# Performance work log

Measured on AMD Instinct MI355X. Metric: run time of the kernel, lower is better.

The kernel has to match this reference:

```python
import jax, jax.numpy as jnp
import numpy as np

B, S, D = 4, 2048, 1024
H, HD = 16, 64
WINDOW = 256


def setup_inputs() -> dict:
    key = jax.random.key(0)
    ks = jax.random.split(key, 5)
    scale = 1.0 / np.sqrt(D)
    return {
        "hidden_states": jax.random.normal(ks[0], (B, S, D), dtype=jnp.float32),
        "Wq": jax.random.normal(ks[1], (D, D), dtype=jnp.float32) * scale,
        "Wk": jax.random.normal(ks[2], (D, D), dtype=jnp.float32) * scale,
        "Wv": jax.random.normal(ks[3], (D, D), dtype=jnp.float32) * scale,
        "Wo": jax.random.normal(ks[4], (D, D), dtype=jnp.float32) * scale,
        "bo": jnp.zeros((D,), dtype=jnp.float32),
    }


def reference(hidden_states, Wq, Wk, Wv, Wo, bo):
    # q/k/v projections (no bias), torch Linear: x @ W.T
    q = hidden_states @ Wq.T  # [B,S,D]
    k = hidden_states @ Wk.T
    v = hidden_states @ Wv.T

    def split_heads(t):  # [B,S,D] -> [B,H,S,HD]
        return t.reshape(B, S, H, HD).transpose(0, 2, 1, 3)

    q, k, v = split_heads(q), split_heads(k), split_heads(v)

    # NOTE: original code does NOT scale by 1/sqrt(head_dim)
    scores = jnp.einsum("bhqd,bhkd->bhqk", q.astype(jnp.float32), k.astype(jnp.float32))

    # local causal band mask: keep j <= i and i - j < WINDOW
    i = jnp.arange(S)[:, None]
    j = jnp.arange(S)[None, :]
    band = (j <= i) & (i - j < WINDOW)  # [S,S] bool
    mask_value = jnp.finfo(scores.dtype).min
    scores = jnp.where(band[None, None, :, :], scores, mask_value)

    attn = jax.nn.softmax(scores, axis=-1).astype(v.dtype)
    ctx = jnp.einsum("bhqk,bhkd->bhqd", attn, v)  # [B,H,S,HD]

    # merge heads -> [B,S,D]
    ctx = ctx.transpose(0, 2, 1, 3).reshape(B, S, D)
    out = ctx @ Wo.T + bo
    return out
```

## Files before the change

kernel.cpp:

```cpp
#include <hip/hip_runtime.h>
#include <hip/hip_bf16.h>
#include <cstdint>
#include <cstddef>

#define S_LEN   2048
#define BATCH   4
#define NHEAD   16
#define HDIM    64
#define DMODEL  1024
#define WIN     256
#define PQ      72

typedef __bf16 bf16x8 __attribute__((ext_vector_type(8)));
typedef float f32x4 __attribute__((ext_vector_type(4)));
typedef unsigned short u16x4 __attribute__((ext_vector_type(4)));
typedef unsigned short u16x8 __attribute__((ext_vector_type(8)));

__device__ __forceinline__ unsigned short f2bf(float x) {
  union { float f; unsigned u; } c; c.f = x;
  unsigned r = (c.u + 0x7fffu + ((c.u >> 16) & 1u)) >> 16;
  return (unsigned short)r;
}

__device__ __forceinline__ void gld_lds16(const void* g, void* l) {
  __builtin_amdgcn_global_load_lds(
      (__attribute__((address_space(1))) void*)g,
      (__attribute__((address_space(3))) void*)l, 16, 0, 0);
}

__global__ __launch_bounds__(256) void convert_kernel(
    const float* __restrict__ s0, const float* __restrict__ s1,
    const float* __restrict__ s2, const float* __restrict__ s3,
    const float* __restrict__ s4,
    unsigned short* __restrict__ d0, unsigned short* __restrict__ d1,
    unsigned short* __restrict__ d2, unsigned short* __restrict__ d3,
    unsigned short* __restrict__ d4) {
  const int z = blockIdx.y;
  const float* s; unsigned short* d; long n;
  if      (z == 0) { s = s0; d = d0; n = (long)8192 * 1024; }
  else if (z == 1) { s = s1; d = d1; n = (long)1024 * 1024; }
  else if (z == 2) { s = s2; d = d2; n = (long)1024 * 1024; }
  else if (z == 3) { s = s3; d = d3; n = (long)1024 * 1024; }
  else             { s = s4; d = d4; n = (long)1024 * 1024; }
  const long base = ((long)blockIdx.x * 256 + threadIdx.x) * 16;
  if (base >= n) return;
#pragma unroll
  for (int i = 0; i < 4; ++i) {
    const float4 f = *(const float4*)(s + base + i * 4);
    u16x4 ov;
    ov.x = f2bf(f.x); ov.y = f2bf(f.y); ov.z = f2bf(f.z); ov.w = f2bf(f.w);
    *(u16x4*)(d + base + i * 4) = ov;
  }
}

template <int MODE>
__device__ __forceinline__ void gemm_pipe_core(
    const unsigned short* __restrict__ A, const unsigned short* __restrict__ B,
    void* __restrict__ C, const float* __restrict__ bias,
    int M, int N, int K, unsigned short* __restrict__ ls) {
  const int m0 = blockIdx.x * 128;
  const int n0 = blockIdx.y * 256;
  const int tid  = threadIdx.x;
  const int lane = tid & 63;
  const int wid  = tid >> 6;
  const int quad = lane >> 4, l16 = lane & 15;
  const int wm = wid >> 2, wn = wid & 3;

  const int REG = 24576;

  const int srow   = tid >> 3;
  const int schunk = tid & 7;
  const int scol   = ((schunk ^ ((tid >> 4) & 7)) << 3);

  f32x4 acc[4][4];
#pragma unroll
  for (int i = 0; i < 4; ++i)
#pragma unroll
    for (int j = 0; j < 4; ++j) acc[i][j] = f32x4{0.f, 0.f, 0.f, 0.f};

  const int NT = K >> 6;

#pragma unroll
  for (int tt = 0; tt < 2; ++tt) {
    const int k0 = tt << 6;
#pragma unroll
    for (int q = 0; q < 2; ++q) {
      const int row = srow + 64 * q;
      gld_lds16(A + (size_t)(m0 + row) * K + k0 + scol,
                ls + tt * REG + row * 64 + schunk * 8);
    }
#pragma unroll
    for (int q = 0; q < 4; ++q) {
      const int row = srow + 64 * q;
      gld_lds16(B + (size_t)(n0 + row) * K + k0 + scol,
                ls + tt * REG + 8192 + row * 64 + schunk * 8);
    }
  }
  asm volatile("s_waitcnt vmcnt(6)" ::: "memory");
  __builtin_amdgcn_s_barrier();
  __builtin_amdgcn_sched_barrier(0);

  for (int t = 0; t < NT; ++t) {
    const int rt = t % 3;
    const unsigned short* la = ls + rt * REG;
    const unsigned short* lb = la + 8192;
    const int ts = t + 2;
    const int rs = ts % 3;
    const bool doStage = ts < NT;
    const int k0s = ts << 6;
    unsigned short* da = ls + rs * REG;

    {
      bf16x8 af[4], bfr[4];
#pragma unroll
      for (int mi = 0; mi < 4; ++mi)
        af[mi] = *(const bf16x8*)(la + (wm * 64 + mi * 16 + l16) * 64 +
                                  ((quad ^ (l16 >> 1)) << 3));
#pragma unroll
      for (int ni = 0; ni < 4; ++ni)
        bfr[ni] = *(const bf16x8*)(lb + (wn * 64 + ni * 16 + l16) * 64 +
                                   ((quad ^ (l16 >> 1)) << 3));
      if (doStage) {
#pragma unroll
        for (int q = 0; q < 2; ++q) {
          const int row = srow + 64 * q;
          gld_lds16(A + (size_t)(m0 + row) * K + k0s + scol,
                    da + row * 64 + schunk * 8);
        }
        gld_lds16(B + (size_t)(n0 + srow) * K + k0s + scol,
                  da + 8192 + srow * 64 + schunk * 8);
      }
      __builtin_amdgcn_s_setprio(1);
#pragma unroll
      for (int mi = 0; mi < 4; ++mi)
#pragma unroll
        for (int ni = 0; ni < 4; ++ni)
          acc[mi][ni] = __builtin_amdgcn_mfma_f32_16x16x32_bf16(
              af[mi], bfr[ni], acc[mi][ni], 0, 0, 0);
      __builtin_amdgcn_s_setprio(0);
    }
    __builtin_amdgcn_s_barrier();
    __builtin_amdgcn_sched_barrier(0);

    {
      bf16x8 af[4], bfr[4];
#pragma unroll
      for (int mi = 0; mi < 4; ++mi)
        af[mi] = *(const bf16x8*)(la + (wm * 64 + mi * 16 + l16) * 64 +
                                  (((4 + quad) ^ (l16 >> 1)) << 3));
#pragma unroll
      for (int ni = 0; ni < 4; ++ni)
        bfr[ni] = *(const bf16x8*)(lb + (wn * 64 + ni * 16 + l16) * 64 +
                                   (((4 + quad) ^ (l16 >> 1)) << 3));
      if (doStage) {
#pragma unroll
        for (int q = 1; q < 4; ++q) {
          const int row = srow + 64 * q;
          gld_lds16(B + (size_t)(n0 + row) * K + k0s + scol,
                    da + 8192 + row * 64 + schunk * 8);
        }
      }
      __builtin_amdgcn_s_setprio(1);
#pragma unroll
      for (int mi = 0; mi < 4; ++mi)
#pragma unroll
        for (int ni = 0; ni < 4; ++ni)
          acc[mi][ni] = __builtin_amdgcn_mfma_f32_16x16x32_bf16(
              af[mi], bfr[ni], acc[mi][ni], 0, 0, 0);
      __builtin_amdgcn_s_setprio(0);
    }
    if (t + 2 < NT) {
      asm volatile("s_waitcnt vmcnt(6)" ::: "memory");
    } else if (t + 1 < NT) {
      asm volatile("s_waitcnt vmcnt(0)" ::: "memory");
    }
    __builtin_amdgcn_s_barrier();
    __builtin_amdgcn_sched_barrier(0);
  }

#pragma unroll
  for (int mi = 0; mi < 4; ++mi) {
    if (MODE == 2) {
      const int mB = m0 + wm * 64 + mi * 16 + quad * 4;
      const int bq = mB >> 11, s = mB & 2047;
#pragma unroll
      for (int ni = 0; ni < 4; ++ni) {
        const int n = n0 + wn * 64 + ni * 16 + l16;
        u16x4 w;
        w[0] = f2bf(acc[mi][ni][0]); w[1] = f2bf(acc[mi][ni][1]);
        w[2] = f2bf(acc[mi][ni][2]); w[3] = f2bf(acc[mi][ni][3]);
        *(u16x4*)((unsigned short*)C +
                  (((size_t)((bq << 4) | (n >> 6)) * 64 + (n & 63)) << 11) + s) = w;
      }
    } else {
#pragma unroll
      for (int r = 0; r < 4; ++r) {
        const int m = m0 + wm * 64 + mi * 16 + quad * 4 + r;
#pragma unroll
        for (int ni = 0; ni < 4; ++ni) {
          const int n = n0 + wn * 64 + ni * 16 + l16;
          const float vv = acc[mi][ni][r];
          if (MODE == 0) {
            ((unsigned short*)C)[(size_t)m * N + n] = f2bf(vv);
          } else {
            ((float*)C)[(size_t)m * N + n] = vv + bias[n];
          }
        }
      }
    }
  }
}

__global__ __launch_bounds__(512, 2) void gemm_qkv_kernel(
    const unsigned short* __restrict__ A,
    const unsigned short* __restrict__ B0, const unsigned short* __restrict__ B1,
    const unsigned short* __restrict__ B2,
    unsigned short* __restrict__ C0, unsigned short* __restrict__ C1,
    unsigned short* __restrict__ Cv, int M, int N, int K) {
  __shared__ unsigned short ls[3 * 24576];
  if (blockIdx.z == 2) {
    gemm_pipe_core<2>(A, B2, Cv, nullptr, M, N, K, ls);
  } else {
    const unsigned short* B = blockIdx.z == 0 ? B0 : B1;
    unsigned short*       C = blockIdx.z == 0 ? C0 : C1;
    gemm_pipe_core<0>(A, B, C, nullptr, M, N, K, ls);
  }
}

template <int MODE>
__device__ __forceinline__ void gemm_bt_core(
    const unsigned short* __restrict__ A, const unsigned short* __restrict__ B,
    void* __restrict__ C, const float* __restrict__ bias,
    int M, int N, int K,
    unsigned short* __restrict__ lsA, unsigned short* __restrict__ lsB) {
  const int m0 = blockIdx.x * 128;
  const int n0 = blockIdx.y * 128;
  const int tid  = threadIdx.x;
  const int wave = tid >> 6, lane = tid & 63;
  const int quad = lane >> 4, l16 = lane & 15;
  const int wm = wave >> 1, wn = wave & 1;

  f32x4 acc[4][4];
#pragma unroll
  for (int i = 0; i < 4; ++i)
#pragma unroll
    for (int j = 0; j < 4; ++j) acc[i][j] = f32x4{0.f, 0.f, 0.f, 0.f};

  const int trow   = tid >> 3;
  const int tchunk = tid & 7;
  const int swz_w  = (trow >> 1) & 7;
  const int scol   = ((tchunk ^ swz_w) << 3);
  const int swz_r  = (l16 >> 1) & 7;

  for (int k0 = 0; k0 < K; k0 += 64) {
    __syncthreads();
#pragma unroll
    for (int c = 0; c < 4; ++c) {
      const int row  = trow + 32 * c;
      const int flat = row * 64 + tchunk * 8;
      gld_lds16(A + (size_t)(m0 + row) * K + k0 + scol, lsA + flat);
      gld_lds16(B + (size_t)(n0 + row) * K + k0 + scol, lsB + flat);
    }
    __syncthreads();

#pragma unroll
    for (int s2 = 0; s2 < 2; ++s2) {
      bf16x8 af[4], bfr[4];
#pragma unroll
      for (int mi = 0; mi < 4; ++mi)
        af[mi] = *(const bf16x8*)(lsA + (wm * 64 + mi * 16 + l16) * 64 +
                                  (((s2 * 4 + quad) ^ swz_r) << 3));
#pragma unroll
      for (int ni = 0; ni < 4; ++ni)
        bfr[ni] = *(const bf16x8*)(lsB + (wn * 64 + ni * 16 + l16) * 64 +
                                   (((s2 * 4 + quad) ^ swz_r) << 3));
#pragma unroll
      for (int mi = 0; mi < 4; ++mi)
#pragma unroll
        for (int ni = 0; ni < 4; ++ni)
          acc[mi][ni] = __builtin_amdgcn_mfma_f32_16x16x32_bf16(
              af[mi], bfr[ni], acc[mi][ni], 0, 0, 0);
    }
  }

#pragma unroll
  for (int mi = 0; mi < 4; ++mi) {
#pragma unroll
    for (int r = 0; r < 4; ++r) {
      const int m = m0 + wm * 64 + mi * 16 + quad * 4 + r;
#pragma unroll
      for (int ni = 0; ni < 4; ++ni) {
        const int n = n0 + wn * 64 + ni * 16 + l16;
        const float vv = acc[mi][ni][r];
        if (MODE == 0) {
          ((unsigned short*)C)[(size_t)m * N + n] = f2bf(vv);
        } else {
          ((float*)C)[(size_t)m * N + n] = vv + bias[n];
        }
      }
    }
  }
}

__global__ __launch_bounds__(256) void gemm_out_kernel(
    const unsigned short* __restrict__ A, const unsigned short* __restrict__ B,
    float* __restrict__ C, const float* __restrict__ bias, int M, int N, int K) {
  __shared__ unsigned short lsA[128 * 64];
  __shared__ unsigned short lsB[128 * 64];
  gemm_bt_core<1>(A, B, C, bias, M, N, K, lsA, lsB);
}

__global__ __launch_bounds__(256) void attn_kernel(
    const unsigned short* __restrict__ q, const unsigned short* __restrict__ k,
    const unsigned short* __restrict__ vt, unsigned short* __restrict__ ctx) {
  const int bh = blockIdx.y;
  const int b = bh >> 4, h = bh & 15;
  const int i0 = blockIdx.x * 128;
  const int tid  = threadIdx.x;
  const int wave = tid >> 6, lane = tid & 63;
  const int quad = lane >> 4, l16 = lane & 15;

  __shared__ unsigned short lsQ[128 * PQ];
  __shared__ unsigned short lsK[64 * PQ];
  __shared__ unsigned short lsVp[64 * PQ];

  {
    const int r = tid >> 1, cb = (tid & 1) * 32;
    const unsigned short* src =
        q + ((size_t)(b * S_LEN + i0 + r) * DMODEL + h * HDIM + cb);
    *(u16x8*)(lsQ + r * PQ + cb)      = *(const u16x8*)src;
    *(u16x8*)(lsQ + r * PQ + cb + 8)  = *(const u16x8*)(src + 8);
    *(u16x8*)(lsQ + r * PQ + cb + 16) = *(const u16x8*)(src + 16);
    *(u16x8*)(lsQ + r * PQ + cb + 24) = *(const u16x8*)(src + 24);
  }

  const int rr = tid >> 2, cb = (tid & 3) * 16;
  const int jhi  = cb >> 4;
  const int vbase = (jhi >> 1) * 32 + (jhi & 1) * 4;

  const int jb0 = (i0 >= WIN) ? ((i0 - WIN + 1) >> 6) : 0;
  const int jb1 = (i0 + 127) >> 6;
  const int jbi = i0 >> 6;

  u16x8 pk0, pk1, pv0, pv1;
  {
    const int j0 = jb0 * 64;
    const unsigned short* ks =
        k + ((size_t)(b * S_LEN + j0 + rr) * DMODEL + h * HDIM + cb);
    pk0 = *(const u16x8*)ks;
    pk1 = *(const u16x8*)(ks + 8);
    const unsigned short* vs =
        vt + ((size_t)(bh * HDIM + rr) * S_LEN + j0 + cb);
    pv0 = *(const u16x8*)vs;
    pv1 = *(const u16x8*)(vs + 8);
  }

  __syncthreads();

  bf16x8 aq[2][2];
#pragma unroll
  for (int t = 0; t < 2; ++t)
#pragma unroll
    for (int s2 = 0; s2 < 2; ++s2)
      aq[t][s2] = *(const bf16x8*)(lsQ + (wave * 32 + t * 16 + l16) * PQ +
                                   s2 * 32 + quad * 8);

  float l_lane[2] = {0.f, 0.f};
  f32x4 o[2][4];
#pragma unroll
  for (int t = 0; t < 2; ++t)
#pragma unroll
    for (int nd = 0; nd < 4; ++nd) o[t][nd] = f32x4{0.f, 0.f, 0.f, 0.f};

  for (int jb = jb0; jb <= jb1; ++jb) {
    const int j0 = jb * 64;
    const bool needMask = !(jb == jbi - 1 || jb == jbi - 2);
    __syncthreads();
    {
      *(u16x8*)(lsK + rr * PQ + cb)     = pk0;
      *(u16x8*)(lsK + rr * PQ + cb + 8) = pk1;
      u16x4 w0, w1, w2, w3;
      w0[0]=pv0[0]; w0[1]=pv0[1]; w0[2]=pv0[2]; w0[3]=pv0[3];
      w1[0]=pv0[4]; w1[1]=pv0[5]; w1[2]=pv0[6]; w1[3]=pv0[7];
      w2[0]=pv1[0]; w2[1]=pv1[1]; w2[2]=pv1[2]; w2[3]=pv1[3];
      w3[0]=pv1[4]; w3[1]=pv1[5]; w3[2]=pv1[6]; w3[3]=pv1[7];
      *(u16x4*)(lsVp + rr * PQ + vbase)      = w0;
      *(u16x4*)(lsVp + rr * PQ + vbase + 8)  = w1;
      *(u16x4*)(lsVp + rr * PQ + vbase + 16) = w2;
      *(u16x4*)(lsVp + rr * PQ + vbase + 24) = w3;
    }
    __syncthreads();

    if (jb < jb1) {
      const int jn = j0 + 64;
      const unsigned short* ks =
          k + ((size_t)(b * S_LEN + jn + rr) * DMODEL + h * HDIM + cb);
      pk0 = *(const u16x8*)ks;
      pk1 = *(const u16x8*)(ks + 8);
      const unsigned short* vs =
          vt + ((size_t)(bh * HDIM + rr) * S_LEN + jn + cb);
      pv0 = *(const u16x8*)vs;
      pv1 = *(const u16x8*)(vs + 8);
    }

    f32x4 st[2][4];
#pragma unroll
    for (int t = 0; t < 2; ++t)
#pragma unroll
      for (int ni = 0; ni < 4; ++ni) st[t][ni] = f32x4{0.f, 0.f, 0.f, 0.f};
    __builtin_amdgcn_s_setprio(1);
#pragma unroll
    for (int s2 = 0; s2 < 2; ++s2) {
      bf16x8 bk[4];
#pragma unroll
      for (int ni = 0; ni < 4; ++ni)
        bk[ni] = *(const bf16x8*)(lsK + (ni * 16 + l16) * PQ + s2 * 32 + quad * 8);
#pragma unroll
      for (int t = 0; t < 2; ++t)
#pragma unroll
        for (int ni = 0; ni < 4; ++ni)
          st[t][ni] = __builtin_amdgcn_mfma_f32_16x16x32_bf16(
              bk[ni], aq[t][s2], st[t][ni], 0, 0, 0);
    }
    __builtin_amdgcn_s_setprio(0);

    bf16x8 ap[2][2];
#pragma unroll
    for (int t = 0; t < 2; ++t) {
      const int iq = i0 + wave * 32 + t * 16 + l16;
      if (needMask) {
#pragma unroll
        for (int ni = 0; ni < 4; ++ni)
#pragma unroll
          for (int r = 0; r < 4; ++r) {
            const int j = j0 + ni * 16 + quad * 4 + r;
            const bool ok = ((unsigned)(iq - j) < (unsigned)WIN);
            const float p = ok ? __expf(fminf(st[t][ni][r], 80.f)) : 0.f;
            st[t][ni][r] = p;
            l_lane[t] += p;
          }
      } else {
#pragma unroll
        for (int ni = 0; ni < 4; ++ni)
#pragma unroll
          for (int r = 0; r < 4; ++r) {
            const float p = __expf(fminf(st[t][ni][r], 80.f));
            st[t][ni][r] = p;
            l_lane[t] += p;
          }
      }
#pragma unroll
      for (int s2 = 0; s2 < 2; ++s2) {
        bf16x8 a;
#pragma unroll
        for (int r = 0; r < 4; ++r) {
          union { unsigned short u; __bf16 h; } c0, c1;
          c0.u = f2bf(st[t][2 * s2][r]);
          c1.u = f2bf(st[t][2 * s2 + 1][r]);
          a[r]     = c0.h;
          a[4 + r] = c1.h;
        }
        ap[t][s2] = a;
      }
    }

    __builtin_amdgcn_s_setprio(1);
#pragma unroll
    for (int s2 = 0; s2 < 2; ++s2) {
      bf16x8 bv[4];
#pragma unroll
      for (int nd = 0; nd < 4; ++nd)
        bv[nd] = *(const bf16x8*)(lsVp + (nd * 16 + l16) * PQ + s2 * 32 + quad * 8);
#pragma unroll
      for (int t = 0; t < 2; ++t)
#pragma unroll
        for (int nd = 0; nd < 4; ++nd)
          o[t][nd] = __builtin_amdgcn_mfma_f32_16x16x32_bf16(
              ap[t][s2], bv[nd], o[t][nd], 0, 0, 0);
    }
    __builtin_amdgcn_s_setprio(0);
  }

#pragma unroll
  for (int t = 0; t < 2; ++t) {
    float l = l_lane[t];
    l += __shfl_xor(l, 16, 64);
    l += __shfl_xor(l, 32, 64);
    const float invl = 1.f / l;
#pragma unroll
    for (int r = 0; r < 4; ++r) {
      const float inv = __shfl(invl, quad * 4 + r, 64);
      const int i = i0 + wave * 32 + t * 16 + quad * 4 + r;
#pragma unroll
      for (int nd = 0; nd < 4; ++nd)
        ctx[(size_t)(b * S_LEN + i) * DMODEL + h * HDIM + nd * 16 + l16] =
            f2bf(o[t][nd][r] * inv);
    }
  }
}

extern "C" void kernel_launch(void* const* d_in, const int* in_sizes, int n_in,
                              void* d_out, int out_size, void* d_ws, size_t ws_size,
                              hipStream_t stream) {
  const float* hs = (const float*)d_in[0];
  const float* Wq = (const float*)d_in[1];
  const float* Wk = (const float*)d_in[2];
  const float* Wv = (const float*)d_in[3];
  const float* Wo = (const float*)d_in[4];
  const float* bo = (const float*)d_in[5];
  float* out = (float*)d_out;

  const size_t MD = (size_t)8192 * 1024;
  const size_t DD = (size_t)1024 * 1024;
  unsigned short* hsb  = (unsigned short*)d_ws;
  unsigned short* wqb  = hsb + MD;
  unsigned short* wkb  = wqb + DD;
  unsigned short* wvb  = wkb + DD;
  unsigned short* wob  = wvb + DD;
  unsigned short* qb   = wob + DD;
  unsigned short* kb   = qb + MD;
  unsigned short* vtb  = kb + MD;
  unsigned short* ctxb = vtb + MD;

  convert_kernel<<<dim3(2048, 5), 256, 0, stream>>>(hs, Wq, Wk, Wv, Wo,
                                                    hsb, wqb, wkb, wvb, wob);
  gemm_qkv_kernel<<<dim3(64, 4, 3), 512, 0, stream>>>(hsb, wqb, wkb, wvb,
                                                      qb, kb, vtb, 8192, 1024, 1024);
  attn_kernel<<<dim3(16, 64), 256, 0, stream>>>(qb, kb, vtb, ctxb);
  gemm_out_kernel<<<dim3(64, 8), 256, 0, stream>>>(ctxb, wob, out, bo,
                                                   8192, 1024, 1024);
}
```

Measured before the change: 215.9 us.

## Enlarge QKV GEMM tile to 256x256 with double-buffered LDS pipeline

The QKV projection GEMM now computes a 256x256 output tile per block instead of 128x256, so each wave holds 8x4 accumulator fragments and B fragments are reused across twice as many A rows. The three-stage, two-tiles-ahead LDS ring is replaced by a two-buffer scheme that prefetches one K-tile ahead, with a full vmcnt(0) wait each iteration. This halves the grid to 384 blocks and raises register and LDS use per block (128 KB LDS), which can reduce occupancy and weaken load/compute overlap.

```diff
diff --git a/kernel.cpp b/kernel.cpp
--- a/kernel.cpp
+++ b/kernel.cpp
@@ -58,7 +58,7 @@
     const unsigned short* __restrict__ A, const unsigned short* __restrict__ B,
     void* __restrict__ C, const float* __restrict__ bias,
     int M, int N, int K, unsigned short* __restrict__ ls) {
-  const int m0 = blockIdx.x * 128;
+  const int m0 = blockIdx.x * 256;
   const int n0 = blockIdx.y * 256;
   const int tid  = threadIdx.x;
   const int lane = tid & 63;
@@ -66,122 +66,105 @@
   const int quad = lane >> 4, l16 = lane & 15;
   const int wm = wid >> 2, wn = wid & 3;
 
-  const int REG = 24576;
+  const int REG = 32768;
 
   const int srow   = tid >> 3;
   const int schunk = tid & 7;
   const int scol   = ((schunk ^ ((tid >> 4) & 7)) << 3);
-
-  f32x4 acc[4][4];
-#pragma unroll
-  for (int i = 0; i < 4; ++i)
+  const int swz_r  = (l16 >> 1) & 7;
+
+  f32x4 acc[8][4];
+#pragma unroll
+  for (int i = 0; i < 8; ++i)
 #pragma unroll
     for (int j = 0; j < 4; ++j) acc[i][j] = f32x4{0.f, 0.f, 0.f, 0.f};
 
   const int NT = K >> 6;
 
 #pragma unroll
-  for (int tt = 0; tt < 2; ++tt) {
-    const int k0 = tt << 6;
-#pragma unroll
-    for (int q = 0; q < 2; ++q) {
-      const int row = srow + 64 * q;
-      gld_lds16(A + (size_t)(m0 + row) * K + k0 + scol,
-                ls + tt * REG + row * 64 + schunk * 8);
-    }
-#pragma unroll
-    for (int q = 0; q < 4; ++q) {
-      const int row = srow + 64 * q;
-      gld_lds16(B + (size_t)(n0 + row) * K + k0 + scol,
-                ls + tt * REG + 8192 + row * 64 + schunk * 8);
-    }
-  }
-  asm volatile("s_waitcnt vmcnt(6)" ::: "memory");
+  for (int q = 0; q < 4; ++q) {
+    const int row = srow + 64 * q;
+    gld_lds16(A + (size_t)(m0 + row) * K + scol, ls + row * 64 + schunk * 8);
+  }
+#pragma unroll
+  for (int q = 0; q < 4; ++q) {
+    const int row = srow + 64 * q;
+    gld_lds16(B + (size_t)(n0 + row) * K + scol,
+              ls + 16384 + row * 64 + schunk * 8);
+  }
+  asm volatile("s_waitcnt vmcnt(0)" ::: "memory");
   __builtin_amdgcn_s_barrier();
   __builtin_amdgcn_sched_barrier(0);
 
   for (int t = 0; t < NT; ++t) {
-    const int rt = t % 3;
-    const unsigned short* la = ls + rt * REG;
-    const unsigned short* lb = la + 8192;
-    const int ts = t + 2;
-    const int rs = ts % 3;
-    const bool doStage = ts < NT;
-    const int k0s = ts << 6;
-    unsigned short* da = ls + rs * REG;
-
-    {
-      bf16x8 af[4], bfr[4];
+    const unsigned short* la = ls + (t & 1) * REG;
+    const unsigned short* lb = la + 16384;
+    unsigned short* da = ls + ((t + 1) & 1) * REG;
+    const bool doStage = (t + 1) < NT;
+    const int k0s = (t + 1) << 6;
+
+    if (doStage) {
+#pragma unroll
+      for (int q = 0; q < 4; ++q) {
+        const int row = srow + 64 * q;
+        gld_lds16(A + (size_t)(m0 + row) * K + k0s + scol,
+                  da + row * 64 + schunk * 8);
+      }
+#pragma unroll
+      for (int q = 0; q < 4; ++q) {
+        const int row = srow + 64 * q;
+        gld_lds16(B + (size_t)(n0 + row) * K + k0s + scol,
+                  da + 16384 + row * 64 + schunk * 8);
+      }
+    }
+
+#pragma unroll
+    for (int s2 = 0; s2 < 2; ++s2) {
+      const int rc = ((s2 * 4 + quad) ^ swz_r) << 3;
+      bf16x8 bfr[4], afl[4];
+#pragma unroll
+      for (int ni = 0; ni < 4; ++ni)
+        bfr[ni] = *(const bf16x8*)(lb + (wn * 64 + ni * 16 + l16) * 64 + rc);
 #pragma unroll
       for (int mi = 0; mi < 4; ++mi)
-        af[mi] = *(const bf16x8*)(la + (wm * 64 + mi * 16 + l16) * 64 +
-                                  ((quad ^ (l16 >> 1)) << 3));
-#pragma unroll
-      for (int ni = 0; ni < 4; ++ni)
-        bfr[ni] = *(const bf16x8*)(lb + (wn * 64 + ni * 16 + l16) * 64 +
-                                   ((quad ^ (l16 >> 1)) << 3));
-      if (doStage) {
-#pragma unroll
-        for (int q = 0; q < 2; ++q) {
-          const int row = srow + 64 * q;
-          gld_lds16(A + (size_t)(m0 + row) * K + k0s + scol,
-                    da + row * 64 + schunk * 8);
-        }
-        gld_lds16(B + (size_t)(n0 + srow) * K + k0s + scol,
-                  da + 8192 + srow * 64 + schunk * 8);
-      }
+        afl[mi] = *(const bf16x8*)(la + (wm * 128 + mi * 16 + l16) * 64 + rc);
+      __builtin_amdgcn_s_barrier();
+      __builtin_amdgcn_sched_barrier(0);
       __builtin_amdgcn_s_setprio(1);
 #pragma unroll
       for (int mi = 0; mi < 4; ++mi)
 #pragma unroll
         for (int ni = 0; ni < 4; ++ni)
           acc[mi][ni] = __builtin_amdgcn_mfma_f32_16x16x32_bf16(
-              af[mi], bfr[ni], acc[mi][ni], 0, 0, 0);
+              afl[mi], bfr[ni], acc[mi][ni], 0, 0, 0);
       __builtin_amdgcn_s_setprio(0);
-    }
-    __builtin_amdgcn_s_barrier();
-    __builtin_amdgcn_sched_barrier(0);
-
-    {
-      bf16x8 af[4], bfr[4];
+
 #pragma unroll
       for (int mi = 0; mi < 4; ++mi)
-        af[mi] = *(const bf16x8*)(la + (wm * 64 + mi * 16 + l16) * 64 +
-                                  (((4 + quad) ^ (l16 >> 1)) << 3));
-#pragma unroll
-      for (int ni = 0; ni < 4; ++ni)
-        bfr[ni] = *(const bf16x8*)(lb + (wn * 64 + ni * 16 + l16) * 64 +
-                                   (((4 + quad) ^ (l16 >> 1)) << 3));
-      if (doStage) {
-#pragma unroll
-        for (int q = 1; q < 4; ++q) {
-          const int row = srow + 64 * q;
-          gld_lds16(B + (size_t)(n0 + row) * K + k0s + scol,
-                    da + 8192 + row * 64 + schunk * 8);
-        }
-      }
+        afl[mi] = *(const bf16x8*)(la + (wm * 128 + (mi + 4) * 16 + l16) * 64 + rc);
+      __builtin_amdgcn_s_barrier();
+      __builtin_amdgcn_sched_barrier(0);
       __builtin_amdgcn_s_setprio(1);
 #pragma unroll
       for (int mi = 0; mi < 4; ++mi)
 #pragma unroll
         for (int ni = 0; ni < 4; ++ni)
-          acc[mi][ni] = __builtin_amdgcn_mfma_f32_16x16x32_bf16(
-              af[mi], bfr[ni], acc[mi][ni], 0, 0, 0);
+          acc[mi + 4][ni] = __builtin_amdgcn_mfma_f32_16x16x32_bf16(
+              afl[mi], bfr[ni], acc[mi + 4][ni], 0, 0, 0);
       __builtin_amdgcn_s_setprio(0);
     }
-    if (t + 2 < NT) {
-      asm volatile("s_waitcnt vmcnt(6)" ::: "memory");
-    } else if (t + 1 < NT) {
+
+    if (doStage) {
       asm volatile("s_waitcnt vmcnt(0)" ::: "memory");
-    }
-    __builtin_amdgcn_s_barrier();
-    __builtin_amdgcn_sched_barrier(0);
-  }
-
-#pragma unroll
-  for (int mi = 0; mi < 4; ++mi) {
+      __builtin_amdgcn_s_barrier();
+      __builtin_amdgcn_sched_barrier(0);
+    }
+  }
+
+#pragma unroll
+  for (int mi = 0; mi < 8; ++mi) {
     if (MODE == 2) {
-      const int mB = m0 + wm * 64 + mi * 16 + quad * 4;
+      const int mB = m0 + wm * 128 + mi * 16 + quad * 4;
       const int bq = mB >> 11, s = mB & 2047;
 #pragma unroll
       for (int ni = 0; ni < 4; ++ni) {
@@ -195,7 +178,7 @@
     } else {
 #pragma unroll
       for (int r = 0; r < 4; ++r) {
-        const int m = m0 + wm * 64 + mi * 16 + quad * 4 + r;
+        const int m = m0 + wm * 128 + mi * 16 + quad * 4 + r;
 #pragma unroll
         for (int ni = 0; ni < 4; ++ni) {
           const int n = n0 + wn * 64 + ni * 16 + l16;
@@ -217,7 +200,7 @@
     const unsigned short* __restrict__ B2,
     unsigned short* __restrict__ C0, unsigned short* __restrict__ C1,
     unsigned short* __restrict__ Cv, int M, int N, int K) {
-  __shared__ unsigned short ls[3 * 24576];
+  __shared__ unsigned short ls[2 * 32768];
   if (blockIdx.z == 2) {
     gemm_pipe_core<2>(A, B2, Cv, nullptr, M, N, K, ls);
   } else {
@@ -524,7 +507,7 @@
 
   convert_kernel<<<dim3(2048, 5), 256, 0, stream>>>(hs, Wq, Wk, Wv, Wo,
                                                     hsb, wqb, wkb, wvb, wob);
-  gemm_qkv_kernel<<<dim3(64, 4, 3), 512, 0, stream>>>(hsb, wqb, wkb, wvb,
+  gemm_qkv_kernel<<<dim3(32, 4, 3), 512, 0, stream>>>(hsb, wqb, wkb, wvb,
                                                       qb, kb, vtb, 8192, 1024, 1024);
   attn_kernel<<<dim3(16, 64), 256, 0, stream>>>(qb, kb, vtb, ctxb);
   gemm_out_kernel<<<dim3(64, 8), 256, 0, stream>>>(ctxb, wob, out, bo,
```

Result: no change. 220.0 us (+1.9%).
